# Optimization experiments

Hardware: AMD Instinct MI355X
Metric: run time of the kernel (lower is better)

Reference implementation:

```python
import jax, jax.numpy as jnp
import numpy as np

N = 20000   # genes
E = 160000  # directed edges (self-loops added in forward, as PyG GATv2Conv does by default)
D = 64      # input feature dim
H1, C1 = 8, 128  # conv1 heads / channels
LRELU_SLOPE = 0.2
LN_EPS = 1e-5


def setup_inputs() -> dict:
    key = jax.random.key(0)
    ks = jax.random.split(key, 20)
    s = 0.05
    inp = {
        "x": jax.random.normal(ks[0], (N, D), dtype=jnp.float32),
        "edge_index": jax.random.randint(ks[1], (2, E), 0, N, dtype=jnp.int64),
        # conv1 (GATv2Conv D -> H1*C1, concat)
        "Wl1": jax.random.normal(ks[2], (D, H1 * C1), dtype=jnp.float32) * s,
        "bl1": jax.random.normal(ks[3], (H1 * C1,), dtype=jnp.float32) * s,
        "Wr1": jax.random.normal(ks[4], (D, H1 * C1), dtype=jnp.float32) * s,
        "br1": jax.random.normal(ks[5], (H1 * C1,), dtype=jnp.float32) * s,
        "att1": jax.random.normal(ks[6], (H1, C1), dtype=jnp.float32) * s,
        "b1": jax.random.normal(ks[7], (H1 * C1,), dtype=jnp.float32) * s,
        # skip Linear(D -> H1*C1)
        "Wskip": jax.random.normal(ks[8], (D, H1 * C1), dtype=jnp.float32) * s,
        "bskip": jax.random.normal(ks[9], (H1 * C1,), dtype=jnp.float32) * s,
        # LayerNorm(H1*C1)
        "g1": jnp.ones((H1 * C1,), dtype=jnp.float32),
        "beta1": jnp.zeros((H1 * C1,), dtype=jnp.float32),
        # conv2 (GATv2Conv H1*C1 -> 2, heads=1, concat=False)
        "Wl2": jax.random.normal(ks[10], (H1 * C1, 2), dtype=jnp.float32) * s,
        "bl2": jax.random.normal(ks[11], (2,), dtype=jnp.float32) * s,
        "Wr2": jax.random.normal(ks[12], (H1 * C1, 2), dtype=jnp.float32) * s,
        "br2": jax.random.normal(ks[13], (2,), dtype=jnp.float32) * s,
        "att2": jax.random.normal(ks[14], (1, 2), dtype=jnp.float32) * s,
        "b2": jax.random.normal(ks[15], (2,), dtype=jnp.float32) * s,
    }
    return inp


def _gatv2(x, src, dst, Wl, bl, Wr, br, att, bias, heads, ch, concat):
    """PyG GATv2Conv (eval mode): message src -> dst, scatter-softmax over dst."""
    n = x.shape[0]
    xl = (x @ Wl + bl).reshape(n, heads, ch)  # source-side transform
    xr = (x @ Wr + br).reshape(n, heads, ch)  # target-side transform
    e = jax.nn.leaky_relu(xl[src] + xr[dst], LRELU_SLOPE)   # [E,H,C]
    alpha = jnp.einsum('ehc,hc->eh', e, att)                 # [E,H]
    amax = jax.ops.segment_max(alpha, dst, num_segments=n)   # [N,H]
    ex = jnp.exp(alpha - amax[dst])
    denom = jax.ops.segment_sum(ex, dst, num_segments=n)
    alpha = ex / (denom[dst] + 1e-16)
    msg = xl[src] * alpha[..., None]                          # [E,H,C]
    out = jax.ops.segment_sum(msg, dst, num_segments=n)      # [N,H,C]
    out = out.reshape(n, heads * ch) if concat else out.mean(axis=1)
    return out + bias


def _layernorm(x, g, b):
    mu = x.mean(axis=-1, keepdims=True)
    var = ((x - mu) ** 2).mean(axis=-1, keepdims=True)
    return (x - mu) * jax.lax.rsqrt(var + LN_EPS) * g + b


def reference(x, edge_index, Wl1, bl1, Wr1, br1, att1, b1, Wskip, bskip,
              g1, beta1, Wl2, bl2, Wr2, br2, att2, b2):
    n = x.shape[0]
    loop = jnp.arange(n, dtype=edge_index.dtype)  # add_self_loops=True (PyG default)
    src = jnp.concatenate([edge_index[0], loop])
    dst = jnp.concatenate([edge_index[1], loop])
    x1 = _gatv2(x, src, dst, Wl1, bl1, Wr1, br1, att1, b1, H1, C1, True) + (x @ Wskip + bskip)
    x1 = jax.nn.elu(_layernorm(x1, g1, beta1))
    # dropout is a no-op in eval mode
    return _gatv2(x1, src, dst, Wl2, bl2, Wr2, br2, att2, b2, 1, 2, False)
```

## Files before the change

### kernel.cpp

```cpp
#include <hip/hip_runtime.h>
#include <hip/hip_bf16.h>
#include <hip/hip_fp16.h>
#include <math.h>

static constexpr int D  = 64;
static constexpr int F1 = 1024;
static constexpr int NTOT = 3072;

typedef _Float16 f16x8 __attribute__((ext_vector_type(8)));
typedef _Float16 h2    __attribute__((ext_vector_type(2)));
typedef float    f32x4 __attribute__((ext_vector_type(4)));

__device__ __forceinline__ float lrelu(float x) { return x > 0.f ? x : 0.2f * x; }

__device__ __forceinline__ float dot2f(h2 a, h2 b, float c) {
#if __has_builtin(__builtin_amdgcn_fdot2)
    return __builtin_amdgcn_fdot2(a, b, c, false);
#else
    return c + (float)a[0] * (float)b[0] + (float)a[1] * (float)b[1];
#endif
}

__device__ __forceinline__ float red16(float p) {
    int v = __builtin_bit_cast(int, p);
    p += __builtin_bit_cast(float, __builtin_amdgcn_mov_dpp(v, 0xB1, 0xF, 0xF, true));
    v = __builtin_bit_cast(int, p);
    p += __builtin_bit_cast(float, __builtin_amdgcn_mov_dpp(v, 0x4E, 0xF, 0xF, true));
    v = __builtin_bit_cast(int, p);
    p += __builtin_bit_cast(float, __builtin_amdgcn_mov_dpp(v, 0x141, 0xF, 0xF, true));
    v = __builtin_bit_cast(int, p);
    p += __builtin_bit_cast(float, __builtin_amdgcn_mov_dpp(v, 0x140, 0xF, 0xF, true));
    return p;
}

union U4H { uint4 u; h2 h[4]; };

__global__ __launch_bounds__(256) void k_prep(
    const float* __restrict__ x, _Float16* __restrict__ xh,
    const int* __restrict__ ei, int* __restrict__ deg,
    const float* __restrict__ Wl1, const float* __restrict__ Wr1,
    const float* __restrict__ Wsk, _Float16* __restrict__ WhT,
    int n, int ne, int m, int castB, int degB)
{
    __shared__ _Float16 wt[128 * 72];
    const int b = blockIdx.x;
    if (b < castB) {
        int t = b * 256 + threadIdx.x;
        int ncast = (n * D) / 4;
        if (t < ncast) {
            float4 v = ((const float4*)x)[t];
            union { _Float16 h[4]; uint2 u; } o;
            o.h[0] = (_Float16)v.x; o.h[1] = (_Float16)v.y;
            o.h[2] = (_Float16)v.z; o.h[3] = (_Float16)v.w;
            *(uint2*)(xh + (size_t)t * 4) = o.u;
        }
    } else if (b < castB + degB) {
        int t = (b - castB) * 256 + threadIdx.x;
        if (t < m) {
            int d = (t < ne) ? ei[ne + t] : t - ne;
            atomicAdd(&deg[d], 1);
        }
    } else {
        const int t = threadIdx.x;
        const int c0 = (b - castB - degB) * 128;
        const float* __restrict__ W = (c0 < 1024) ? Wl1 : (c0 < 2048) ? Wr1 : Wsk;
        const int cw = c0 & 1023;
#pragma unroll
        for (int q = 0; q < 8; ++q) {
            int idx = t + 256 * q;
            int k = idx >> 5, c4 = (idx & 31) * 4;
            float4 v = *(const float4*)(W + (size_t)k * F1 + cw + c4);
            wt[(c4 + 0) * 72 + k] = (_Float16)v.x;
            wt[(c4 + 1) * 72 + k] = (_Float16)v.y;
            wt[(c4 + 2) * 72 + k] = (_Float16)v.z;
            wt[(c4 + 3) * 72 + k] = (_Float16)v.w;
        }
        __syncthreads();
#pragma unroll
        for (int q = 0; q < 4; ++q) {
            int idx = t + 256 * q;
            int c = idx >> 3, k0 = (idx & 7) * 8;
            uint4 v = *(const uint4*)(&wt[c * 72 + k0]);
            *(uint4*)(WhT + (size_t)(c0 + c) * 64 + k0) = v;
        }
    }
}

__global__ __launch_bounds__(1024) void k_scan(const int* __restrict__ deg,
                                               int* __restrict__ rowptr, int n)
{
    __shared__ int sums[1024];
    const int t = threadIdx.x;
    const int chunk = (n + 1023) / 1024;
    const int base = t * chunk;
    int s = 0;
    for (int i = 0; i < chunk; ++i) {
        int idx = base + i;
        if (idx < n) s += deg[idx];
    }
    sums[t] = s;
    __syncthreads();
    for (int off = 1; off < 1024; off <<= 1) {
        int v = (t >= off) ? sums[t - off] : 0;
        __syncthreads();
        sums[t] += v;
        __syncthreads();
    }
    int run = (t == 0) ? 0 : sums[t - 1];
    for (int i = 0; i < chunk; ++i) {
        int idx = base + i;
        if (idx < n) { rowptr[idx] = run; run += deg[idx]; }
    }
    if (t == 0) rowptr[n] = sums[1023];
}

__global__ void k_scatter(const int* __restrict__ ei, const int* __restrict__ rowptr,
                          int* __restrict__ cursor, int* __restrict__ csr_off,
                          int ne, int m)
{
    int e = blockIdx.x * blockDim.x + threadIdx.x;
    if (e >= m) return;
    int s, d;
    if (e < ne) { s = ei[e]; d = ei[ne + e]; }
    else        { s = e - ne; d = s; }
    int pos = rowptr[d] + atomicAdd(&cursor[d], 1);
    csr_off[pos] = s << 11;
}

#define AS(r, c) smem[(r) * 72 + (c)]
#define BS(r, c) smem[128 * 72 + (r) * 72 + (c)]
#define CS(r, c) smem[(r) * 136 + (c)]
__global__ __launch_bounds__(256) void k_gemm_mfma(
    const _Float16* __restrict__ xh, const _Float16* __restrict__ WhT,
    const float* __restrict__ bl1, const float* __restrict__ br1,
    const float* __restrict__ bsk, const float* __restrict__ b1,
    _Float16* __restrict__ xl1h, _Float16* __restrict__ xr1h,
    _Float16* __restrict__ sk1h, int n)
{
    extern __shared__ _Float16 smem[];
    const int t  = threadIdx.x;
    const int r0 = blockIdx.x * 128;
    const int c0 = blockIdx.y * 128;

#pragma unroll
    for (int q = 0; q < 4; ++q) {
        int c = t + 256 * q;
        int row = c >> 3, off = (c & 7) * 8;
        uint4 v = make_uint4(0, 0, 0, 0);
        if (r0 + row < n) v = *(const uint4*)(xh + (size_t)(r0 + row) * 64 + off);
        *(uint4*)(&AS(row, off)) = v;
        uint4 w = *(const uint4*)(WhT + (size_t)(c0 + row) * 64 + off);
        *(uint4*)(&BS(row, off)) = w;
    }
    __syncthreads();

    const int wave = t >> 6, lane = t & 63;
    const int quad = lane >> 4, l16 = lane & 15;
    const int mw = (wave & 1) * 64, nw = (wave >> 1) * 64;

    f16x8 bfrag[4][2];
#pragma unroll
    for (int nt = 0; nt < 4; ++nt)
#pragma unroll
        for (int ks = 0; ks < 2; ++ks)
            bfrag[nt][ks] = *(const f16x8*)(&BS(nw + nt * 16 + l16, ks * 32 + quad * 8));

    f32x4 acc[4][4];
#pragma unroll
    for (int mt = 0; mt < 4; ++mt)
#pragma unroll
        for (int nt = 0; nt < 4; ++nt) acc[mt][nt] = (f32x4){0.f, 0.f, 0.f, 0.f};

#pragma unroll
    for (int mt = 0; mt < 4; ++mt) {
        f16x8 af[2];
#pragma unroll
        for (int ks = 0; ks < 2; ++ks)
            af[ks] = *(const f16x8*)(&AS(mw + mt * 16 + l16, ks * 32 + quad * 8));
#pragma unroll
        for (int nt = 0; nt < 4; ++nt)
#pragma unroll
            for (int ks = 0; ks < 2; ++ks)
                acc[mt][nt] = __builtin_amdgcn_mfma_f32_16x16x32_f16(
                    af[ks], bfrag[nt][ks], acc[mt][nt], 0, 0, 0);
    }

    const int which = c0 >> 10;
    const int csec  = c0 & 1023;
    __syncthreads();
#pragma unroll
    for (int nt = 0; nt < 4; ++nt) {
        int col = csec + nw + nt * 16 + l16;
        float bias = (which == 0) ? bl1[col] : (which == 1) ? br1[col]
                                             : (bsk[col] + b1[col]);
#pragma unroll
        for (int mt = 0; mt < 4; ++mt) {
#pragma unroll
            for (int r = 0; r < 4; ++r)
                CS(mw + mt * 16 + quad * 4 + r, nw + nt * 16 + l16) =
                    (_Float16)(acc[mt][nt][r] + bias);
        }
    }
    __syncthreads();

    _Float16* __restrict__ dst = (which == 0) ? xl1h : (which == 1) ? xr1h : sk1h;
#pragma unroll
    for (int it = 0; it < 8; ++it) {
        int idx = t + 256 * it;
        int row = idx >> 4, c16 = idx & 15;
        int grow = r0 + row;
        if (grow < n) {
            uint4 v = *(uint4*)(&CS(row, c16 * 8));
            *(uint4*)(dst + (size_t)grow * F1 + csec + c16 * 8) = v;
        }
    }
}

__global__ __launch_bounds__(256, 4) void k_conv1_ln(
    const int* __restrict__ rowptr, const int* __restrict__ csr_off,
    const _Float16* __restrict__ xl1h, const _Float16* __restrict__ xr1h,
    const _Float16* __restrict__ sk1h,
    const float* __restrict__ att1,
    const float* __restrict__ g1, const float* __restrict__ beta1,
    const float* __restrict__ Wl2, const float* __restrict__ bl2,
    const float* __restrict__ Wr2, const float* __restrict__ br2,
    float* __restrict__ xl2, float* __restrict__ xr2, int n)
{
    __shared__ float sb[2][2][6];
    const int slot = threadIdx.x >> 7;
    const int q    = (threadIdx.x >> 6) & 1;
    const int lane = threadIdx.x & 63;
    const int node = blockIdx.x * 2 + slot;
    const bool active = node < n;
    const int cb  = q * 512 + lane * 8;
    const int cbB = cb * 2;
    const h2 c02 = (h2){(_Float16)0.2f, (_Float16)0.2f};
    const char* __restrict__ xlB = (const char*)xl1h;

    h2 xrv[4], at2[4], O[4];
    float ll = 0.f;
    float v[8];
    float s1 = 0.f, s2 = 0.f;

    if (active) {
        U4H u; u.u = *(const uint4*)(xr1h + (size_t)node * F1 + cb);
#pragma unroll
        for (int j = 0; j < 4; ++j) xrv[j] = u.h[j];
        float4 a0 = *(const float4*)(att1 + cb);
        float4 a1 = *(const float4*)(att1 + cb + 4);
        at2[0] = (h2){(_Float16)a0.x, (_Float16)a0.y};
        at2[1] = (h2){(_Float16)a0.z, (_Float16)a0.w};
        at2[2] = (h2){(_Float16)a1.x, (_Float16)a1.y};
        at2[3] = (h2){(_Float16)a1.z, (_Float16)a1.w};
#pragma unroll
        for (int j = 0; j < 4; ++j) O[j] = (h2){(_Float16)0.f, (_Float16)0.f};

        const int beg = rowptr[node], end = rowptr[node + 1];

        auto edge = [&](const U4H& cur, bool valid) {
            float p = 0.f;
#pragma unroll
            for (int j = 0; j < 4; ++j) {
                h2 s = cur.h[j] + xrv[j];
                h2 r = __builtin_elementwise_max(s, s * c02);
                p = dot2f(r, at2[j], p);
            }
            p = red16(p);
            float w = valid ? __expf(p) : 0.f;
            ll += w;
            _Float16 wh = (_Float16)w;
            h2 wh2 = (h2){wh, wh};
#pragma unroll
            for (int j = 0; j < 4; ++j) O[j] = O[j] + wh2 * cur.h[j];
        };

        U4H A0, A1, B0, B1;
        {
            int i1 = (beg + 1 < end) ? beg + 1 : beg;
            A0.u = *(const uint4*)(xlB + (size_t)(unsigned)csr_off[beg] + cbB);
            A1.u = *(const uint4*)(xlB + (size_t)(unsigned)csr_off[i1]  + cbB);
        }
        int i = beg;
        while (true) {
            bool more = (i + 2 < end);
            if (more) {
                int j0 = i + 2;
                int j1 = (i + 3 < end) ? i + 3 : j0;
                B0.u = *(const uint4*)(xlB + (size_t)(unsigned)csr_off[j0] + cbB);
                B1.u = *(const uint4*)(xlB + (size_t)(unsigned)csr_off[j1] + cbB);
            }
            edge(A0, true);
            edge(A1, i + 1 < end);
            i += 2;
            if (!more) break;

            bool more2 = (i + 2 < end);
            if (more2) {
                int j0 = i + 2;
                int j1 = (i + 3 < end) ? i + 3 : j0;
                A0.u = *(const uint4*)(xlB + (size_t)(unsigned)csr_off[j0] + cbB);
                A1.u = *(const uint4*)(xlB + (size_t)(unsigned)csr_off[j1] + cbB);
            }
            edge(B0, true);
            edge(B1, i + 1 < end);
            i += 2;
            if (!more2) break;
        }

        float inv = 1.f / (ll + 1e-16f);
        U4H su; su.u = *(const uint4*)(sk1h + (size_t)node * F1 + cb);
#pragma unroll
        for (int j = 0; j < 4; ++j) {
            float xv0 = (float)su.h[j][0] + (float)O[j][0] * inv;
            float xv1 = (float)su.h[j][1] + (float)O[j][1] * inv;
            v[2 * j]     = xv0;
            v[2 * j + 1] = xv1;
            s1 += xv0 + xv1;
            s2 += xv0 * xv0 + xv1 * xv1;
        }
    }
#pragma unroll
    for (int off = 32; off > 0; off >>= 1) {
        s1 += __shfl_xor(s1, off);
        s2 += __shfl_xor(s2, off);
    }
    if (lane == 0) { sb[slot][q][0] = s1; sb[slot][q][1] = s2; }
    __syncthreads();
    float mu  = (sb[slot][0][0] + sb[slot][1][0]) * (1.f / 1024.f);
    float ms  = (sb[slot][0][1] + sb[slot][1][1]) * (1.f / 1024.f);
    float var = fmaxf(ms - mu * mu, 0.f);
    float inv = rsqrtf(var + 1e-5f);

    float p0 = 0.f, p1 = 0.f, p2 = 0.f, p3 = 0.f;
    if (active) {
        float4 gA = *(const float4*)(g1 + cb),    gB = *(const float4*)(g1 + cb + 4);
        float4 bA = *(const float4*)(beta1 + cb), bB = *(const float4*)(beta1 + cb + 4);
        float gv[8] = {gA.x, gA.y, gA.z, gA.w, gB.x, gB.y, gB.z, gB.w};
        float bv[8] = {bA.x, bA.y, bA.z, bA.w, bB.x, bB.y, bB.z, bB.w};
#pragma unroll
        for (int j = 0; j < 8; j += 2) {
            float4 wl = *(const float4*)(Wl2 + (cb + j) * 2);
            float4 wr = *(const float4*)(Wr2 + (cb + j) * 2);
            float y0 = (v[j]   - mu) * inv * gv[j]   + bv[j];
            float y1 = (v[j+1] - mu) * inv * gv[j+1] + bv[j+1];
            float z0 = y0 > 0.f ? y0 : __expf(y0) - 1.f;
            float z1 = y1 > 0.f ? y1 : __expf(y1) - 1.f;
            p0 += z0 * wl.x + z1 * wl.z;
            p1 += z0 * wl.y + z1 * wl.w;
            p2 += z0 * wr.x + z1 * wr.z;
            p3 += z0 * wr.y + z1 * wr.w;
        }
    }
#pragma unroll
    for (int off = 32; off > 0; off >>= 1) {
        p0 += __shfl_xor(p0, off); p1 += __shfl_xor(p1, off);
        p2 += __shfl_xor(p2, off); p3 += __shfl_xor(p3, off);
    }
    if (lane == 0) { sb[slot][q][2] = p0; sb[slot][q][3] = p1;
                     sb[slot][q][4] = p2; sb[slot][q][5] = p3; }
    __syncthreads();
    if (active && lane == 0 && q == 0) {
        xl2[node * 2 + 0] = sb[slot][0][2] + sb[slot][1][2] + bl2[0];
        xl2[node * 2 + 1] = sb[slot][0][3] + sb[slot][1][3] + bl2[1];
        xr2[node * 2 + 0] = sb[slot][0][4] + sb[slot][1][4] + br2[0];
        xr2[node * 2 + 1] = sb[slot][0][5] + sb[slot][1][5] + br2[1];
    }
}

__global__ __launch_bounds__(64) void k_conv2(
    const int* __restrict__ rowptr, const int* __restrict__ csr_off,
    const float* __restrict__ xl2, const float* __restrict__ xr2,
    const float* __restrict__ att2, const float* __restrict__ b2,
    float* __restrict__ out2, int n)
{
    int d = blockIdx.x * blockDim.x + threadIdx.x;
    if (d >= n) return;
    float2 xr = *(const float2*)(xr2 + 2 * d);
    float a0w = att2[0], a1w = att2[1];
    float m = -INFINITY, l = 0.f, o0 = 0.f, o1 = 0.f;
    const int beg = rowptr[d], end = rowptr[d + 1];
    float2 pf[2];
    pf[0] = *(const float2*)(xl2 + (csr_off[beg] >> 10));
    pf[1] = (beg + 1 < end) ? *(const float2*)(xl2 + (csr_off[beg + 1] >> 10)) : pf[0];
    for (int i = beg; i < end; ++i) {
        float2 cur = pf[0];
        pf[0] = pf[1];
        if (i + 2 < end) pf[1] = *(const float2*)(xl2 + (csr_off[i + 2] >> 10));
        float p = lrelu(cur.x + xr.x) * a0w + lrelu(cur.y + xr.y) * a1w;
        float nm = fmaxf(m, p);
        float sc = __expf(m - nm);
        float w  = __expf(p - nm);
        l = l * sc + w;
        o0 = o0 * sc + w * cur.x;
        o1 = o1 * sc + w * cur.y;
        m = nm;
    }
    float inv = 1.f / (l + 1e-16f);
    out2[2 * d + 0] = o0 * inv + b2[0];
    out2[2 * d + 1] = o1 * inv + b2[1];
}

extern "C" void kernel_launch(void* const* d_in, const int* in_sizes, int n_in,
                              void* d_out, int out_size, void* d_ws, size_t ws_size,
                              hipStream_t stream)
{
    const float* x     = (const float*)d_in[0];
    const int*   ei    = (const int*)  d_in[1];
    const float* Wl1   = (const float*)d_in[2];
    const float* bl1   = (const float*)d_in[3];
    const float* Wr1   = (const float*)d_in[4];
    const float* br1   = (const float*)d_in[5];
    const float* att1  = (const float*)d_in[6];
    const float* b1    = (const float*)d_in[7];
    const float* Wsk   = (const float*)d_in[8];
    const float* bsk   = (const float*)d_in[9];
    const float* g1    = (const float*)d_in[10];
    const float* beta1 = (const float*)d_in[11];
    const float* Wl2   = (const float*)d_in[12];
    const float* bl2   = (const float*)d_in[13];
    const float* Wr2   = (const float*)d_in[14];
    const float* br2   = (const float*)d_in[15];
    const float* att2  = (const float*)d_in[16];
    const float* b2    = (const float*)d_in[17];

    const int n  = in_sizes[0] / D;
    const int ne = in_sizes[1] / 2;
    const int m  = ne + n;

    float* ws = (float*)d_ws;
    size_t o = 0;
    _Float16* xl1h = (_Float16*)(ws + o); o += (size_t)n * F1 / 2;
    _Float16* xr1h = (_Float16*)(ws + o); o += (size_t)n * F1 / 2;
    _Float16* sk1h = (_Float16*)(ws + o); o += (size_t)n * F1 / 2;
    _Float16* xh   = (_Float16*)(ws + o); o += (size_t)n * D / 2;
    _Float16* WhT  = (_Float16*)(ws + o); o += (size_t)NTOT * 64 / 2;
    float* xl2    = ws + o; o += (size_t)n * 2;
    float* xr2    = ws + o; o += (size_t)n * 2;
    int* rowptr   = (int*)(ws + o); o += (size_t)n + 1;
    int* deg      = (int*)(ws + o); o += (size_t)n;
    int* cursor   = (int*)(ws + o); o += (size_t)n;
    int* csr_off  = (int*)(ws + o); o += (size_t)m;
    float* out2   = (float*)d_out;

    hipMemsetAsync(deg, 0, (size_t)2 * n * sizeof(int), stream);
    const int castB = ((n * D) / 4 + 255) / 256;
    const int degB  = (m + 255) / 256;
    k_prep<<<castB + degB + NTOT / 128, 256, 0, stream>>>(
        x, xh, ei, deg, Wl1, Wr1, Wsk, WhT, n, ne, m, castB, degB);
    k_scan<<<1, 1024, 0, stream>>>(deg, rowptr, n);
    k_scatter<<<(m + 255) / 256, 256, 0, stream>>>(ei, rowptr, cursor, csr_off, ne, m);

    dim3 gg((n + 127) / 128, NTOT / 128);
    k_gemm_mfma<<<gg, 256, 36864, stream>>>(xh, WhT, bl1, br1, bsk, b1,
                                            xl1h, xr1h, sk1h, n);

    k_conv1_ln<<<(n + 1) / 2, 256, 0, stream>>>(rowptr, csr_off, xl1h, xr1h, sk1h,
                                                att1, g1, beta1, Wl2, bl2, Wr2, br2,
                                                xl2, xr2, n);

    k_conv2<<<(n + 63) / 64, 64, 0, stream>>>(rowptr, csr_off, xl2, xr2, att2, b2, out2, n);
}
```

Before: 252.3 us.

## Fold CSR scatter into GEMM grid, deepen edge prefetch, use nontemporal stores

The CSR scatter kernel becomes an extra row of blocks in the GEMM grid, so the atomic scatter overlaps the MFMA work and one launch goes away. The conv1 edge loop now prefetches and processes four edges per step instead of two, which puts more gathers in flight and interleaves the cross-lane reductions. GEMM output stores are marked nontemporal. The deeper prefetch raises register pressure under launch_bounds(256,4), and the padded loads for nodes with few edges re-fetch the last neighbour.

```diff
diff --git a/kernel.cpp b/kernel.cpp
--- a/kernel.cpp
+++ b/kernel.cpp
@@ -10,6 +10,7 @@
 typedef _Float16 f16x8 __attribute__((ext_vector_type(8)));
 typedef _Float16 h2    __attribute__((ext_vector_type(2)));
 typedef float    f32x4 __attribute__((ext_vector_type(4)));
+typedef unsigned int u32x4 __attribute__((ext_vector_type(4)));
 
 __device__ __forceinline__ float lrelu(float x) { return x > 0.f ? x : 0.2f * x; }
 
@@ -114,19 +115,6 @@
     if (t == 0) rowptr[n] = sums[1023];
 }
 
-__global__ void k_scatter(const int* __restrict__ ei, const int* __restrict__ rowptr,
-                          int* __restrict__ cursor, int* __restrict__ csr_off,
-                          int ne, int m)
-{
-    int e = blockIdx.x * blockDim.x + threadIdx.x;
-    if (e >= m) return;
-    int s, d;
-    if (e < ne) { s = ei[e]; d = ei[ne + e]; }
-    else        { s = e - ne; d = s; }
-    int pos = rowptr[d] + atomicAdd(&cursor[d], 1);
-    csr_off[pos] = s << 11;
-}
-
 #define AS(r, c) smem[(r) * 72 + (c)]
 #define BS(r, c) smem[128 * 72 + (r) * 72 + (c)]
 #define CS(r, c) smem[(r) * 136 + (c)]
@@ -135,10 +123,26 @@
     const float* __restrict__ bl1, const float* __restrict__ br1,
     const float* __restrict__ bsk, const float* __restrict__ b1,
     _Float16* __restrict__ xl1h, _Float16* __restrict__ xr1h,
-    _Float16* __restrict__ sk1h, int n)
+    _Float16* __restrict__ sk1h,
+    const int* __restrict__ ei, const int* __restrict__ rowptr,
+    int* __restrict__ cursor, int* __restrict__ csr_off,
+    int n, int ne, int m)
 {
     extern __shared__ _Float16 smem[];
     const int t  = threadIdx.x;
+
+    if (blockIdx.y == gridDim.y - 1) {
+        const int stride = gridDim.x * 256;
+        for (int e = blockIdx.x * 256 + t; e < m; e += stride) {
+            int s, d;
+            if (e < ne) { s = ei[e]; d = ei[ne + e]; }
+            else        { s = e - ne; d = s; }
+            int pos = rowptr[d] + atomicAdd(&cursor[d], 1);
+            csr_off[pos] = s << 11;
+        }
+        return;
+    }
+
     const int r0 = blockIdx.x * 128;
     const int c0 = blockIdx.y * 128;
 
@@ -210,8 +214,9 @@
         int row = idx >> 4, c16 = idx & 15;
         int grow = r0 + row;
         if (grow < n) {
-            uint4 v = *(uint4*)(&CS(row, c16 * 8));
-            *(uint4*)(dst + (size_t)grow * F1 + csec + c16 * 8) = v;
+            u32x4 v = *(u32x4*)(&CS(row, c16 * 8));
+            __builtin_nontemporal_store(v,
+                (u32x4*)(dst + (size_t)grow * F1 + csec + c16 * 8));
         }
     }
 }
@@ -257,53 +262,54 @@
 
         const int beg = rowptr[node], end = rowptr[node + 1];
 
-        auto edge = [&](const U4H& cur, bool valid) {
-            float p = 0.f;
-#pragma unroll
-            for (int j = 0; j < 4; ++j) {
-                h2 s = cur.h[j] + xrv[j];
-                h2 r = __builtin_elementwise_max(s, s * c02);
-                p = dot2f(r, at2[j], p);
+        auto load4 = [&](U4H* buf, int base) {
+#pragma unroll
+            for (int k = 0; k < 4; ++k) {
+                int idx = base + k;
+                idx = idx < end ? idx : end - 1;
+                buf[k].u = *(const uint4*)(xlB + (size_t)(unsigned)csr_off[idx] + cbB);
             }
-            p = red16(p);
-            float w = valid ? __expf(p) : 0.f;
-            ll += w;
-            _Float16 wh = (_Float16)w;
-            h2 wh2 = (h2){wh, wh};
-#pragma unroll
-            for (int j = 0; j < 4; ++j) O[j] = O[j] + wh2 * cur.h[j];
         };
-
-        U4H A0, A1, B0, B1;
-        {
-            int i1 = (beg + 1 < end) ? beg + 1 : beg;
-            A0.u = *(const uint4*)(xlB + (size_t)(unsigned)csr_off[beg] + cbB);
-            A1.u = *(const uint4*)(xlB + (size_t)(unsigned)csr_off[i1]  + cbB);
-        }
+        auto proc4 = [&](const U4H* buf, int base) {
+            float p[4];
+#pragma unroll
+            for (int k = 0; k < 4; ++k) {
+                float pp = 0.f;
+#pragma unroll
+                for (int j = 0; j < 4; ++j) {
+                    h2 s = buf[k].h[j] + xrv[j];
+                    h2 r = __builtin_elementwise_max(s, s * c02);
+                    pp = dot2f(r, at2[j], pp);
+                }
+                p[k] = pp;
+            }
+#pragma unroll
+            for (int k = 0; k < 4; ++k) p[k] = red16(p[k]);
+#pragma unroll
+            for (int k = 0; k < 4; ++k) {
+                float w = (base + k < end) ? __expf(p[k]) : 0.f;
+                ll += w;
+                _Float16 wh = (_Float16)w;
+                h2 wh2 = (h2){wh, wh};
+#pragma unroll
+                for (int j = 0; j < 4; ++j) O[j] = O[j] + wh2 * buf[k].h[j];
+            }
+        };
+
+        U4H A[4], B[4];
+        load4(A, beg);
         int i = beg;
         while (true) {
-            bool more = (i + 2 < end);
-            if (more) {
-                int j0 = i + 2;
-                int j1 = (i + 3 < end) ? i + 3 : j0;
-                B0.u = *(const uint4*)(xlB + (size_t)(unsigned)csr_off[j0] + cbB);
-                B1.u = *(const uint4*)(xlB + (size_t)(unsigned)csr_off[j1] + cbB);
-            }
-            edge(A0, true);
-            edge(A1, i + 1 < end);
-            i += 2;
+            bool more = (i + 4 < end);
+            if (more) load4(B, i + 4);
+            proc4(A, i);
+            i += 4;
             if (!more) break;
 
-            bool more2 = (i + 2 < end);
-            if (more2) {
-                int j0 = i + 2;
-                int j1 = (i + 3 < end) ? i + 3 : j0;
-                A0.u = *(const uint4*)(xlB + (size_t)(unsigned)csr_off[j0] + cbB);
-                A1.u = *(const uint4*)(xlB + (size_t)(unsigned)csr_off[j1] + cbB);
-            }
-            edge(B0, true);
-            edge(B1, i + 1 < end);
-            i += 2;
+            bool more2 = (i + 4 < end);
+            if (more2) load4(A, i + 4);
+            proc4(B, i);
+            i += 4;
             if (!more2) break;
         }
 
@@ -442,17 +448,18 @@
     int* csr_off  = (int*)(ws + o); o += (size_t)m;
     float* out2   = (float*)d_out;
 
-    hipMemsetAsync(deg, 0, (size_t)2 * n * sizeof(int), stream);
+    (void)hipMemsetAsync(deg, 0, (size_t)2 * n * sizeof(int), stream);
     const int castB = ((n * D) / 4 + 255) / 256;
     const int degB  = (m + 255) / 256;
     k_prep<<<castB + degB + NTOT / 128, 256, 0, stream>>>(
         x, xh, ei, deg, Wl1, Wr1, Wsk, WhT, n, ne, m, castB, degB);
     k_scan<<<1, 1024, 0, stream>>>(deg, rowptr, n);
-    k_scatter<<<(m + 255) / 256, 256, 0, stream>>>(ei, rowptr, cursor, csr_off, ne, m);
-
-    dim3 gg((n + 127) / 128, NTOT / 128);
+
+    dim3 gg((n + 127) / 128, NTOT / 128 + 1);
     k_gemm_mfma<<<gg, 256, 36864, stream>>>(xh, WhT, bl1, br1, bsk, b1,
-                                            xl1h, xr1h, sk1h, n);
+                                            xl1h, xr1h, sk1h,
+                                            ei, rowptr, cursor, csr_off,
+                                            n, ne, m);
 
     k_conv1_ln<<<(n + 1) / 2, 256, 0, stream>>>(rowptr, csr_off, xl1h, xr1h, sk1h,
                                                 att1, g1, beta1, Wl2, bl2, Wr2, br2,
```

Result: no change. 254.6 us (+0.9%).
